# Optimization experiments

Measured on AMD Instinct MI355X. Metric: run time of the kernel, lower is better.

The kernel has to match this reference:

```python
import jax, jax.numpy as jnp
import numpy as np
import math

K_SLOTS = 64
DIM = 512
HEADS = 8
HEAD_DIM = DIM // HEADS
EPS = 1e-20
LN_EPS = 1e-5
SQRT_DIM = 1.0 / math.sqrt(HEAD_DIM)


def layernorm(x, g, b):
    mu = jnp.mean(x, axis=-1, keepdims=True)
    var = jnp.var(x, axis=-1, keepdims=True)
    return (x - mu) * jax.lax.rsqrt(var + LN_EPS) * g + b


def setup_inputs() -> dict:
    key = jax.random.key(0)
    ks = jax.random.split(key, 8)
    B, T = 8, 8192
    lim = 1.0 / math.sqrt(DIM)
    return {
        "X": jax.random.normal(ks[0], (B, T, DIM), jnp.float32),
        "slots_w": jax.random.normal(ks[1], (K_SLOTS, DIM), jnp.float32),
        "g_slots": jnp.ones((DIM,), jnp.float32),
        "b_slots": jnp.zeros((DIM,), jnp.float32),
        "Wk": jax.random.uniform(ks[2], (DIM, DIM), jnp.float32, -lim, lim),
        "bk": jax.random.uniform(ks[3], (DIM,), jnp.float32, -lim, lim),
        "Wv": jax.random.uniform(ks[4], (DIM, DIM), jnp.float32, -lim, lim),
        "bv": jax.random.uniform(ks[5], (DIM,), jnp.float32, -lim, lim),
        "g_after": jnp.ones((DIM,), jnp.float32),
        "b_after": jnp.zeros((DIM,), jnp.float32),
    }


def reference(X, slots_w, g_slots, b_slots, Wk, bk, Wv, bv, g_after, b_after):
    B, T, D = X.shape
    # slots -> queries, shared across batch: (K, D) -> (H, K, hd)
    S = layernorm(slots_w, g_slots, b_slots)
    Q = S.reshape(K_SLOTS, HEADS, HEAD_DIM).transpose(1, 0, 2)  # (H, K, hd)
    # key/value projections, head split: (B, T, D) -> (B, H, T, hd)
    Kx = (X @ Wk.T + bk).reshape(B, T, HEADS, HEAD_DIM).transpose(0, 2, 1, 3)
    V = (X @ Wv.T + bv).reshape(B, T, HEADS, HEAD_DIM).transpose(0, 2, 1, 3)
    # attention logits (B, H, K, T), scale = 1/sqrt(head_dim)
    A = jnp.einsum("hkd,bhsd->bhks", Q, Kx) * SQRT_DIM
    # softmax over the SLOT axis (k), then renormalize by row-sum over s
    W = jax.nn.softmax(A, axis=-2)
    C = jnp.sum(W, axis=-1, keepdims=True)  # (B, H, K, 1)
    A = W / (C + EPS)
    S_hat = jnp.einsum("bhks,bhsd->bhkd", A, V)  # (B, H, K, hd)
    S_hat = S_hat.transpose(0, 2, 1, 3).reshape(B, K_SLOTS, D)
    return layernorm(S_hat, g_after, b_after)
```

## Files before the change

### kernel.cpp

```cpp
#include <hip/hip_runtime.h>
#include <hip/hip_bf16.h>
#include <math.h>

typedef unsigned short ushort_t;
typedef unsigned int u32;

constexpr int D  = 512;
constexpr int T  = 8192;
constexpr int B  = 8;
constexpr int H  = 8;
constexpr int KS = 64;
constexpr int HD = 64;
constexpr float SCALE = 0.125f;
constexpr float LNEPS = 1e-5f;
constexpr float EPS   = 1e-20f;

constexpr int TC  = 128;
constexpr int CPB = 2;

constexpr size_t OFF_S    = 0;
constexpr size_t OFF_BQ   = 32768;
constexpr size_t OFF_SACC = 33280;
constexpr size_t OFF_CACC = 295424;
constexpr size_t OFF_WB2  = 299520;
constexpr size_t OFF_XB   = 561664;
constexpr size_t WS_NEED  = (OFF_XB + (size_t)B*T*D/2) * 4;

typedef __attribute__((ext_vector_type(8))) short bf16x8;
typedef __attribute__((ext_vector_type(4))) float f32x4;
typedef __attribute__((ext_vector_type(4))) unsigned short us4;

typedef const __attribute__((address_space(1))) u32* gas_ptr;
typedef __attribute__((address_space(3))) u32* las_ptr;

__device__ __forceinline__ void gload16(const void* g, void* l) {
  __builtin_amdgcn_global_load_lds((gas_ptr)g, (las_ptr)l, 16, 0, 0);
}

__device__ __forceinline__ ushort_t f2bf(float x) {
  __hip_bfloat16 t = __float2bfloat16(x);
  return *(ushort_t*)&t;
}

__device__ __forceinline__ u32 pk2bf(float x, float y) {
  __hip_bfloat162 t = __float22bfloat162_rn(make_float2(x, y));
  return *(u32*)&t;
}

__device__ __forceinline__ bf16x8 cvt8(f32x4 a, f32x4 b) {
  union { bf16x8 v; u32 u[4]; } r;
  r.u[0] = pk2bf(a.x, a.y); r.u[1] = pk2bf(a.z, a.w);
  r.u[2] = pk2bf(b.x, b.y); r.u[3] = pk2bf(b.z, b.w);
  return r.v;
}

__global__ void ln_slots_kernel(const float* __restrict__ slots_w,
                                const float* __restrict__ g, const float* __restrict__ b,
                                float* __restrict__ S) {
  __shared__ float red[8];
  int k = blockIdx.x;
  int tid = threadIdx.x;
  float x0 = slots_w[k*D + tid];
  float x1 = slots_w[k*D + tid + 256];
  float s1 = x0 + x1, s2 = x0*x0 + x1*x1;
  for (int off = 32; off; off >>= 1) { s1 += __shfl_xor(s1, off); s2 += __shfl_xor(s2, off); }
  if ((tid & 63) == 0) { red[tid >> 6] = s1; red[4 + (tid >> 6)] = s2; }
  __syncthreads();
  s1 = red[0] + red[1] + red[2] + red[3];
  s2 = red[4] + red[5] + red[6] + red[7];
  float mu = s1 / D;
  float var = s2 / D - mu * mu;
  float rs = rsqrtf(var + LNEPS);
  S[k*D + tid]       = (x0 - mu) * rs * g[tid]       + b[tid];
  S[k*D + tid + 256] = (x1 - mu) * rs * g[tid + 256] + b[tid + 256];
}

__global__ void weff_kernel(const float* __restrict__ S, const float* __restrict__ Wk,
                            ushort_t* __restrict__ Wb2) {
  int gid = blockIdx.x * 256 + threadIdx.x;
  int in = gid & 511;
  int hk = gid >> 9;
  int h = hk >> 6, k = hk & 63;
  const float* srow = S + k*D + h*HD;
  const float* wcol = Wk + (size_t)(h*HD)*D + in;
  float acc = 0.f;
  #pragma unroll 8
  for (int d = 0; d < HD; ++d) acc += srow[d] * wcol[(size_t)d*D];
  Wb2[(size_t)(h*128 + k)*D + in] = f2bf(acc * SCALE);
}

__global__ void bq_kernel(const float* __restrict__ S, const float* __restrict__ bk,
                          float* __restrict__ bq) {
  int hk = blockIdx.x * 256 + threadIdx.x;
  int h = hk >> 6, k = hk & 63;
  float acc = 0.f;
  for (int d = 0; d < HD; ++d) acc += S[k*D + h*HD + d] * bk[h*HD + d];
  bq[hk] = acc * SCALE;
}

__global__ void wvcopy_kernel(const float* __restrict__ Wv, ushort_t* __restrict__ Wb2) {
  int gid = blockIdx.x * 256 + threadIdx.x;
  int in = gid & 511;
  int hd = gid >> 9;
  int h = hd >> 6, d = hd & 63;
  Wb2[(size_t)(h*128 + 64 + d)*D + in] = f2bf(Wv[(size_t)hd*D + in]);
}

__global__ void zero_kernel(float* __restrict__ p, int n) {
  int gid = blockIdx.x * 256 + threadIdx.x;
  if (gid < n) p[gid] = 0.f;
}

__global__ void xcvt_kernel(const float* __restrict__ X, ushort_t* __restrict__ Xb) {
  size_t i = ((size_t)blockIdx.x * 256 + threadIdx.x) * 8;
  f32x4 a = *(const f32x4*)(X + i);
  f32x4 b = *(const f32x4*)(X + i + 4);
  *(bf16x8*)(Xb + i) = cvt8(a, b);
}

__global__ __launch_bounds__(256, 4) void main_kernel_bf16(
    const ushort_t* __restrict__ Xb, const ushort_t* __restrict__ Wb2,
    const float* __restrict__ bq, const float* __restrict__ bv,
    float* __restrict__ Sacc, float* __restrict__ Cacc) {
  __shared__ __align__(16) char smem[34816];
  ushort_t* A_lds = (ushort_t*)smem;
  ushort_t* B_lds = (ushort_t*)(smem + 8192);
  ushort_t* W_lds = (ushort_t*)smem;
  ushort_t* V_lds = (ushort_t*)(smem + 17408);

  const int tid  = threadIdx.x;
  const int lane = tid & 63, w = tid >> 6;
  const int wm = w & 1, wn = w >> 1;
  const int m16 = lane & 15, q = lane >> 4;
  const int kq = q ^ ((m16 >> 1) & 3);

  const int id = blockIdx.x;
  const int h  = (id >> 3) & 7;
  const int cg = (id & 7) | ((id >> 6) << 3);
  const int bh = (cg >> 5) * H + h;

  f32x4 acc2[4] = {};
  float csum[4] = {0.f, 0.f, 0.f, 0.f};

  for (int cc = 0; cc < CPB; ++cc) {
    const ushort_t* Xc = Xb + (size_t)(cg * CPB + cc) * TC * D;
    f32x4 acc[4][4] = {};

    for (int kb = 0; kb < D; kb += 32) {
      __syncthreads();
      #pragma unroll
      for (int m = 0; m < 2; ++m) {
        int li = tid + m * 256;
        int row = li >> 2;
        int kc = (li & 3) ^ ((row >> 1) & 3);
        gload16(Xc + (size_t)row * D + kb + kc * 8, A_lds + (size_t)li * 8);
      }
      #pragma unroll
      for (int m = 0; m < 2; ++m) {
        int li = tid + m * 256;
        int col = li >> 2;
        int kc = (li & 3) ^ ((col >> 1) & 3);
        gload16(Wb2 + (size_t)(h * 128 + col) * D + kb + kc * 8, B_lds + (size_t)li * 8);
      }
      __syncthreads();
      bf16x8 af[4], bfv[4];
      #pragma unroll
      for (int i = 0; i < 4; ++i)
        af[i] = *(const bf16x8*)(A_lds + (size_t)(((wm*64 + i*16 + m16) << 2) | kq) * 8);
      #pragma unroll
      for (int j = 0; j < 4; ++j)
        bfv[j] = *(const bf16x8*)(B_lds + (size_t)(((wn*64 + j*16 + m16) << 2) | kq) * 8);
      #pragma unroll
      for (int i = 0; i < 4; ++i)
        #pragma unroll
        for (int j = 0; j < 4; ++j)
          acc[i][j] = __builtin_amdgcn_mfma_f32_16x16x32_bf16(af[i], bfv[j], acc[i][j], 0, 0, 0);
    }
    __syncthreads();

    if (wn == 0) {
      float bqv[4];
      #pragma unroll
      for (int j = 0; j < 4; ++j) bqv[j] = bq[h * KS + j * 16 + m16];
      #pragma unroll
      for (int i = 0; i < 4; ++i) {
        us4 wp[4];
        #pragma unroll
        for (int r = 0; r < 4; ++r) {
          float v0 = acc[i][0][r] + bqv[0];
          float v1 = acc[i][1][r] + bqv[1];
          float v2 = acc[i][2][r] + bqv[2];
          float v3 = acc[i][3][r] + bqv[3];
          float mx = fmaxf(fmaxf(v0, v1), fmaxf(v2, v3));
          mx = fmaxf(mx, __shfl_xor(mx, 1));
          mx = fmaxf(mx, __shfl_xor(mx, 2));
          mx = fmaxf(mx, __shfl_xor(mx, 4));
          mx = fmaxf(mx, __shfl_xor(mx, 8));
          v0 = __expf(v0 - mx); v1 = __expf(v1 - mx);
          v2 = __expf(v2 - mx); v3 = __expf(v3 - mx);
          float s = v0 + v1 + v2 + v3;
          s += __shfl_xor(s, 1); s += __shfl_xor(s, 2);
          s += __shfl_xor(s, 4); s += __shfl_xor(s, 8);
          float inv = __builtin_amdgcn_rcpf(s);
          v0 *= inv; v1 *= inv; v2 *= inv; v3 *= inv;
          csum[0] += v0; csum[1] += v1; csum[2] += v2; csum[3] += v3;
          wp[0][r] = f2bf(v0); wp[1][r] = f2bf(v1);
          wp[2][r] = f2bf(v2); wp[3][r] = f2bf(v3);
        }
        #pragma unroll
        for (int j = 0; j < 4; ++j)
          *(us4*)(W_lds + (j * 16 + m16) * 136 + wm * 64 + i * 16 + q * 4) = wp[j];
      }
    } else {
      float bvv[4];
      #pragma unroll
      for (int j = 0; j < 4; ++j) bvv[j] = bv[h * HD + j * 16 + m16];
      #pragma unroll
      for (int i = 0; i < 4; ++i) {
        #pragma unroll
        for (int j = 0; j < 4; ++j) {
          us4 pk;
          pk.x = f2bf(acc[i][j][0] + bvv[j]);
          pk.y = f2bf(acc[i][j][1] + bvv[j]);
          pk.z = f2bf(acc[i][j][2] + bvv[j]);
          pk.w = f2bf(acc[i][j][3] + bvv[j]);
          *(us4*)(V_lds + (j * 16 + m16) * 136 + wm * 64 + i * 16 + q * 4) = pk;
        }
      }
    }
    __syncthreads();

    #pragma unroll
    for (int kk = 0; kk < 4; ++kk) {
      bf16x8 a = *(const bf16x8*)(W_lds + (w * 16 + m16) * 136 + kk * 32 + q * 8);
      #pragma unroll
      for (int j = 0; j < 4; ++j) {
        bf16x8 bb = *(const bf16x8*)(V_lds + (j * 16 + m16) * 136 + kk * 32 + q * 8);
        acc2[j] = __builtin_amdgcn_mfma_f32_16x16x32_bf16(a, bb, acc2[j], 0, 0, 0);
      }
    }
  }

  float* Sb = Sacc + (size_t)bh * KS * HD;
  #pragma unroll
  for (int j = 0; j < 4; ++j)
    #pragma unroll
    for (int r = 0; r < 4; ++r)
      atomicAdd(Sb + (w * 16 + q * 4 + r) * HD + j * 16 + m16, acc2[j][r]);

  if (wn == 0) {
    #pragma unroll
    for (int j = 0; j < 4; ++j) {
      float c = csum[j];
      c += __shfl_xor(c, 16);
      c += __shfl_xor(c, 32);
      if (q == 0) atomicAdd(Cacc + (size_t)bh * KS + j * 16 + m16, c);
    }
  }
}

__global__ __launch_bounds__(256, 3) void main_kernel_f32(
    const float* __restrict__ X, const ushort_t* __restrict__ Wb2,
    const float* __restrict__ bq, const float* __restrict__ bv,
    float* __restrict__ Sacc, float* __restrict__ Cacc) {
  __shared__ __align__(16) char smem[34816];
  float*    A_lds = (float*)smem;
  ushort_t* B_lds = (ushort_t*)(smem + 16384);
  ushort_t* W_lds = (ushort_t*)smem;
  ushort_t* V_lds = (ushort_t*)(smem + 17408);

  const int tid  = threadIdx.x;
  const int lane = tid & 63, w = tid >> 6;
  const int wm = w & 1, wn = w >> 1;
  const int m16 = lane & 15, q = lane >> 4;

  const int id = blockIdx.x;
  const int h  = (id >> 3) & 7;
  const int cg = (id & 7) | ((id >> 6) << 3);
  const int bh = (cg >> 5) * H + h;

  f32x4 acc2[4] = {};
  float csum[4] = {0.f, 0.f, 0.f, 0.f};

  for (int cc = 0; cc < CPB; ++cc) {
    const float* Xc = X + (size_t)(cg * CPB + cc) * TC * D;
    f32x4 acc[4][4] = {};
    for (int kb = 0; kb < D; kb += 32) {
      __syncthreads();
      #pragma unroll
      for (int m = 0; m < 4; ++m) {
        int li = tid + m * 256;
        int row = li >> 3, c = li & 7;
        gload16(Xc + (size_t)row * D + kb + c * 4, A_lds + (size_t)li * 4);
      }
      #pragma unroll
      for (int m = 0; m < 2; ++m) {
        int li = tid + m * 256;
        int col = li >> 2, c = li & 3;
        gload16(Wb2 + (size_t)(h * 128 + col) * D + kb + c * 8, B_lds + (size_t)li * 8);
      }
      __syncthreads();
      bf16x8 af[4], bfv[4];
      #pragma unroll
      for (int i = 0; i < 4; ++i) {
        const f32x4* ap = (const f32x4*)(A_lds + (wm * 64 + i * 16 + m16) * 32 + q * 8);
        af[i] = cvt8(ap[0], ap[1]);
      }
      #pragma unroll
      for (int j = 0; j < 4; ++j)
        bfv[j] = *(const bf16x8*)(B_lds + (wn * 64 + j * 16 + m16) * 32 + q * 8);
      #pragma unroll
      for (int i = 0; i < 4; ++i)
        #pragma unroll
        for (int j = 0; j < 4; ++j)
          acc[i][j] = __builtin_amdgcn_mfma_f32_16x16x32_bf16(af[i], bfv[j], acc[i][j], 0, 0, 0);
    }
    __syncthreads();

    if (wn == 0) {
      float bqv[4];
      #pragma unroll
      for (int j = 0; j < 4; ++j) bqv[j] = bq[h * KS + j * 16 + m16];
      #pragma unroll
      for (int i = 0; i < 4; ++i) {
        us4 wp[4];
        #pragma unroll
        for (int r = 0; r < 4; ++r) {
          float v0 = acc[i][0][r] + bqv[0];
          float v1 = acc[i][1][r] + bqv[1];
          float v2 = acc[i][2][r] + bqv[2];
          float v3 = acc[i][3][r] + bqv[3];
          float mx = fmaxf(fmaxf(v0, v1), fmaxf(v2, v3));
          mx = fmaxf(mx, __shfl_xor(mx, 1));
          mx = fmaxf(mx, __shfl_xor(mx, 2));
          mx = fmaxf(mx, __shfl_xor(mx, 4));
          mx = fmaxf(mx, __shfl_xor(mx, 8));
          v0 = __expf(v0 - mx); v1 = __expf(v1 - mx);
          v2 = __expf(v2 - mx); v3 = __expf(v3 - mx);
          float s = v0 + v1 + v2 + v3;
          s += __shfl_xor(s, 1); s += __shfl_xor(s, 2);
          s += __shfl_xor(s, 4); s += __shfl_xor(s, 8);
          float inv = __builtin_amdgcn_rcpf(s);
          v0 *= inv; v1 *= inv; v2 *= inv; v3 *= inv;
          csum[0] += v0; csum[1] += v1; csum[2] += v2; csum[3] += v3;
          wp[0][r] = f2bf(v0); wp[1][r] = f2bf(v1);
          wp[2][r] = f2bf(v2); wp[3][r] = f2bf(v3);
        }
        #pragma unroll
        for (int j = 0; j < 4; ++j)
          *(us4*)(W_lds + (j * 16 + m16) * 136 + wm * 64 + i * 16 + q * 4) = wp[j];
      }
    } else {
      float bvv[4];
      #pragma unroll
      for (int j = 0; j < 4; ++j) bvv[j] = bv[h * HD + j * 16 + m16];
      #pragma unroll
      for (int i = 0; i < 4; ++i) {
        #pragma unroll
        for (int j = 0; j < 4; ++j) {
          us4 pk;
          pk.x = f2bf(acc[i][j][0] + bvv[j]);
          pk.y = f2bf(acc[i][j][1] + bvv[j]);
          pk.z = f2bf(acc[i][j][2] + bvv[j]);
          pk.w = f2bf(acc[i][j][3] + bvv[j]);
          *(us4*)(V_lds + (j * 16 + m16) * 136 + wm * 64 + i * 16 + q * 4) = pk;
        }
      }
    }
    __syncthreads();

    #pragma unroll
    for (int kk = 0; kk < 4; ++kk) {
      bf16x8 a = *(const bf16x8*)(W_lds + (w * 16 + m16) * 136 + kk * 32 + q * 8);
      #pragma unroll
      for (int j = 0; j < 4; ++j) {
        bf16x8 bb = *(const bf16x8*)(V_lds + (j * 16 + m16) * 136 + kk * 32 + q * 8);
        acc2[j] = __builtin_amdgcn_mfma_f32_16x16x32_bf16(a, bb, acc2[j], 0, 0, 0);
      }
    }
  }

  float* Sb = Sacc + (size_t)bh * KS * HD;
  #pragma unroll
  for (int j = 0; j < 4; ++j)
    #pragma unroll
    for (int r = 0; r < 4; ++r)
      atomicAdd(Sb + (w * 16 + q * 4 + r) * HD + j * 16 + m16, acc2[j][r]);

  if (wn == 0) {
    #pragma unroll
    for (int j = 0; j < 4; ++j) {
      float c = csum[j];
      c += __shfl_xor(c, 16);
      c += __shfl_xor(c, 32);
      if (q == 0) atomicAdd(Cacc + (size_t)bh * KS + j * 16 + m16, c);
    }
  }
}

__global__ void finalize_kernel(const float* __restrict__ Sacc, const float* __restrict__ Cacc,
                                const float* __restrict__ g, const float* __restrict__ bb,
                                float* __restrict__ out) {
  __shared__ float red[8];
  int bk_ = blockIdx.x;
  int b = bk_ >> 6, k = bk_ & 63;
  int tid = threadIdx.x;
  float v[2];
  #pragma unroll
  for (int m = 0; m < 2; ++m) {
    int d = tid + m*256;
    int h = d >> 6, dd = d & 63;
    float c = Cacc[((size_t)b*H + h)*KS + k];
    v[m] = Sacc[(((size_t)b*H + h)*KS + k)*HD + dd] / (c + EPS);
  }
  float s1 = v[0] + v[1], s2 = v[0]*v[0] + v[1]*v[1];
  for (int off = 32; off; off >>= 1) { s1 += __shfl_xor(s1, off); s2 += __shfl_xor(s2, off); }
  if ((tid & 63) == 0) { red[tid >> 6] = s1; red[4 + (tid >> 6)] = s2; }
  __syncthreads();
  s1 = red[0] + red[1] + red[2] + red[3];
  s2 = red[4] + red[5] + red[6] + red[7];
  float mu = s1 / D;
  float var = s2 / D - mu * mu;
  float rs = rsqrtf(var + LNEPS);
  #pragma unroll
  for (int m = 0; m < 2; ++m) {
    int d = tid + m*256;
    out[(size_t)bk_*D + d] = (v[m] - mu) * rs * g[d] + bb[d];
  }
}

extern "C" void kernel_launch(void* const* d_in, const int* in_sizes, int n_in,
                              void* d_out, int out_size, void* d_ws, size_t ws_size,
                              hipStream_t stream) {
  const float* X       = (const float*)d_in[0];
  const float* slots_w = (const float*)d_in[1];
  const float* g_slots = (const float*)d_in[2];
  const float* b_slots = (const float*)d_in[3];
  const float* Wk      = (const float*)d_in[4];
  const float* bk      = (const float*)d_in[5];
  const float* Wv      = (const float*)d_in[6];
  const float* bv      = (const float*)d_in[7];
  const float* g_after = (const float*)d_in[8];
  const float* b_after = (const float*)d_in[9];
  float* ws   = (float*)d_ws;
  float* S    = ws + OFF_S;
  float* bq   = ws + OFF_BQ;
  float* Sacc = ws + OFF_SACC;
  float* Cacc = ws + OFF_CACC;
  ushort_t* Wb2 = (ushort_t*)(ws + OFF_WB2);
  ushort_t* Xb  = (ushort_t*)(ws + OFF_XB);
  float* out  = (float*)d_out;

  hipLaunchKernelGGL(ln_slots_kernel, dim3(64), dim3(256), 0, stream, slots_w, g_slots, b_slots, S);
  hipLaunchKernelGGL(weff_kernel, dim3(1024), dim3(256), 0, stream, S, Wk, Wb2);
  hipLaunchKernelGGL(bq_kernel, dim3(2), dim3(256), 0, stream, S, bk, bq);
  hipLaunchKernelGGL(wvcopy_kernel, dim3(1024), dim3(256), 0, stream, Wv, Wb2);
  hipLaunchKernelGGL(zero_kernel, dim3(1040), dim3(256), 0, stream, Sacc, 266240);
  if (ws_size >= WS_NEED) {
    hipLaunchKernelGGL(xcvt_kernel, dim3(16384), dim3(256), 0, stream, X, Xb);
    hipLaunchKernelGGL(main_kernel_bf16, dim3(2048), dim3(256), 0, stream,
                       Xb, Wb2, bq, bv, Sacc, Cacc);
  } else {
    hipLaunchKernelGGL(main_kernel_f32, dim3(2048), dim3(256), 0, stream,
                       X, Wb2, bq, bv, Sacc, Cacc);
  }
  hipLaunchKernelGGL(finalize_kernel, dim3(B * KS), dim3(256), 0, stream,
                     Sacc, Cacc, g_after, b_after, out);
}
```

Measured before the change: 416.5 us.

## Keep a bf16 X tile in LDS and process all heads per block

Removes the separate X-to-bf16 conversion pass. A new 512-thread kernel loads each 128-token chunk of fp32 X once, converts it to bf16 into a large swizzled LDS tile (about 144KB of dynamic shared memory), and loops over all 8 heads. B fragments are read directly from global memory with register double-buffering, so X is no longer re-read once per head. The cost is one block per CU with no overlap between the initial X load and compute, plus more barriers in the per-head W·V stage.

New measurement: 416.5 us. Within noise of the previous version (-0.0%).

```diff
diff --git a/kernel.cpp b/kernel.cpp
--- a/kernel.cpp
+++ b/kernel.cpp
@@ -15,16 +15,15 @@
 constexpr float LNEPS = 1e-5f;
 constexpr float EPS   = 1e-20f;
 
-constexpr int TC  = 128;
-constexpr int CPB = 2;
+constexpr int TC = 128;
 
 constexpr size_t OFF_S    = 0;
 constexpr size_t OFF_BQ   = 32768;
 constexpr size_t OFF_SACC = 33280;
 constexpr size_t OFF_CACC = 295424;
 constexpr size_t OFF_WB2  = 299520;
-constexpr size_t OFF_XB   = 561664;
-constexpr size_t WS_NEED  = (OFF_XB + (size_t)B*T*D/2) * 4;
+
+constexpr int MAIN_LDS = 147456;
 
 typedef __attribute__((ext_vector_type(8))) short bf16x8;
 typedef __attribute__((ext_vector_type(4))) float f32x4;
@@ -111,20 +110,174 @@
   if (gid < n) p[gid] = 0.f;
 }
 
-__global__ void xcvt_kernel(const float* __restrict__ X, ushort_t* __restrict__ Xb) {
-  size_t i = ((size_t)blockIdx.x * 256 + threadIdx.x) * 8;
-  f32x4 a = *(const f32x4*)(X + i);
-  f32x4 b = *(const f32x4*)(X + i + 4);
-  *(bf16x8*)(Xb + i) = cvt8(a, b);
-}
-
-__global__ __launch_bounds__(256, 4) void main_kernel_bf16(
-    const ushort_t* __restrict__ Xb, const ushort_t* __restrict__ Wb2,
+__global__ __launch_bounds__(512, 2) void main_kernel_ah(
+    const float* __restrict__ X, const ushort_t* __restrict__ Wb2,
+    const float* __restrict__ bq, const float* __restrict__ bv,
+    float* __restrict__ Sacc, float* __restrict__ Cacc) {
+  extern __shared__ __align__(16) char smem[];
+  ushort_t* X_lds = (ushort_t*)smem;
+  ushort_t* W_lds = (ushort_t*)(smem + 131072);
+  ushort_t* V_lds = (ushort_t*)(smem + 139264);
+
+  const int tid = threadIdx.x;
+  const int w = tid >> 6, lane = tid & 63;
+  const int m16 = lane & 15, q = lane >> 4;
+  const int th = w & 1, cqq = w >> 1;
+  const int bid = blockIdx.x;
+  const int bb = bid >> 6;
+  const float* Xc = X + (size_t)bid * TC * D;
+
+  #pragma unroll
+  for (int m = 0; m < 16; ++m) {
+    int C = m * 512 + tid;
+    int token = C >> 6, c = C & 63;
+    const f32x4* src = (const f32x4*)(Xc + (size_t)C * 8);
+    f32x4 a = src[0], b2 = src[1];
+    *(bf16x8*)(X_lds + ((size_t)token * 64 + (c ^ (token & 7))) * 8) = cvt8(a, b2);
+  }
+  __syncthreads();
+
+  const int hh_my = cqq >> 1;
+  const int isV   = cqq & 1;
+
+  for (int p = 0; p < 4; ++p) {
+    f32x4 acc[4][4] = {};
+    const ushort_t* Bp = Wb2 + ((size_t)((p * 2 + hh_my) * 128 + isV * 64 + m16)) * D + q * 8;
+    bf16x8 bnx[4];
+    #pragma unroll
+    for (int j = 0; j < 4; ++j) bnx[j] = *(const bf16x8*)(Bp + (size_t)j * 16 * D);
+    #pragma unroll 2
+    for (int it = 0; it < 16; ++it) {
+      bf16x8 bc[4];
+      #pragma unroll
+      for (int j = 0; j < 4; ++j) bc[j] = bnx[j];
+      if (it < 15) {
+        #pragma unroll
+        for (int j = 0; j < 4; ++j)
+          bnx[j] = *(const bf16x8*)(Bp + (it + 1) * 32 + (size_t)j * 16 * D);
+      }
+      bf16x8 af[4];
+      #pragma unroll
+      for (int i = 0; i < 4; ++i) {
+        int token = th * 64 + i * 16 + m16;
+        af[i] = *(const bf16x8*)(X_lds + ((size_t)token * 64 + ((it * 4 + q) ^ (token & 7))) * 8);
+      }
+      #pragma unroll
+      for (int i = 0; i < 4; ++i)
+        #pragma unroll
+        for (int j = 0; j < 4; ++j)
+          acc[i][j] = __builtin_amdgcn_mfma_f32_16x16x32_bf16(af[i], bc[j], acc[i][j], 0, 0, 0);
+    }
+
+    for (int hh = 0; hh < 2; ++hh) {
+      const int head = p * 2 + hh;
+      const int bh = bb * 8 + head;
+      const bool mine = (hh_my == hh);
+      us4 pk[4][4];
+      if (mine) {
+        if (!isV) {
+          float bqv[4];
+          #pragma unroll
+          for (int j = 0; j < 4; ++j) bqv[j] = bq[head * 64 + j * 16 + m16];
+          float cs0 = 0.f, cs1 = 0.f, cs2 = 0.f, cs3 = 0.f;
+          #pragma unroll
+          for (int i = 0; i < 4; ++i) {
+            #pragma unroll
+            for (int r = 0; r < 4; ++r) {
+              float v0 = acc[i][0][r] + bqv[0];
+              float v1 = acc[i][1][r] + bqv[1];
+              float v2 = acc[i][2][r] + bqv[2];
+              float v3 = acc[i][3][r] + bqv[3];
+              float mx = fmaxf(fmaxf(v0, v1), fmaxf(v2, v3));
+              mx = fmaxf(mx, __shfl_xor(mx, 1));
+              mx = fmaxf(mx, __shfl_xor(mx, 2));
+              mx = fmaxf(mx, __shfl_xor(mx, 4));
+              mx = fmaxf(mx, __shfl_xor(mx, 8));
+              v0 = __expf(v0 - mx); v1 = __expf(v1 - mx);
+              v2 = __expf(v2 - mx); v3 = __expf(v3 - mx);
+              float s = v0 + v1 + v2 + v3;
+              s += __shfl_xor(s, 1); s += __shfl_xor(s, 2);
+              s += __shfl_xor(s, 4); s += __shfl_xor(s, 8);
+              float inv = __builtin_amdgcn_rcpf(s);
+              v0 *= inv; v1 *= inv; v2 *= inv; v3 *= inv;
+              cs0 += v0; cs1 += v1; cs2 += v2; cs3 += v3;
+              pk[i][0][r] = f2bf(v0); pk[i][1][r] = f2bf(v1);
+              pk[i][2][r] = f2bf(v2); pk[i][3][r] = f2bf(v3);
+            }
+          }
+          cs0 += __shfl_xor(cs0, 16); cs0 += __shfl_xor(cs0, 32);
+          cs1 += __shfl_xor(cs1, 16); cs1 += __shfl_xor(cs1, 32);
+          cs2 += __shfl_xor(cs2, 16); cs2 += __shfl_xor(cs2, 32);
+          cs3 += __shfl_xor(cs3, 16); cs3 += __shfl_xor(cs3, 32);
+          if (q == 0) {
+            atomicAdd(Cacc + (size_t)bh * KS +  0 + m16, cs0);
+            atomicAdd(Cacc + (size_t)bh * KS + 16 + m16, cs1);
+            atomicAdd(Cacc + (size_t)bh * KS + 32 + m16, cs2);
+            atomicAdd(Cacc + (size_t)bh * KS + 48 + m16, cs3);
+          }
+        } else {
+          float bvv[4];
+          #pragma unroll
+          for (int j = 0; j < 4; ++j) bvv[j] = bv[head * 64 + j * 16 + m16];
+          #pragma unroll
+          for (int i = 0; i < 4; ++i)
+            #pragma unroll
+            for (int j = 0; j < 4; ++j) {
+              pk[i][j][0] = f2bf(acc[i][j][0] + bvv[j]);
+              pk[i][j][1] = f2bf(acc[i][j][1] + bvv[j]);
+              pk[i][j][2] = f2bf(acc[i][j][2] + bvv[j]);
+              pk[i][j][3] = f2bf(acc[i][j][3] + bvv[j]);
+            }
+        }
+      }
+
+      f32x4 acc2[2] = {};
+      #pragma unroll
+      for (int half = 0; half < 2; ++half) {
+        __syncthreads();
+        if (mine && th == half) {
+          ushort_t* dst = isV ? V_lds : W_lds;
+          #pragma unroll
+          for (int i = 0; i < 4; ++i)
+            #pragma unroll
+            for (int j = 0; j < 4; ++j) {
+              int rowv = j * 16 + m16;
+              int tc = i * 2 + (q >> 1);
+              *(us4*)(dst + ((size_t)rowv * 8 + (tc ^ (rowv & 7))) * 8 + (q & 1) * 4) = pk[i][j];
+            }
+        }
+        __syncthreads();
+        #pragma unroll
+        for (int ks = 0; ks < 2; ++ks) {
+          int tcc = ks * 4 + q;
+          int sl = (w & 3) * 16 + m16;
+          bf16x8 a2 = *(const bf16x8*)(W_lds + ((size_t)sl * 8 + (tcc ^ (m16 & 7))) * 8);
+          #pragma unroll
+          for (int jj = 0; jj < 2; ++jj) {
+            int dm = (w >> 2) * 32 + jj * 16 + m16;
+            bf16x8 b2v = *(const bf16x8*)(V_lds + ((size_t)dm * 8 + (tcc ^ (m16 & 7))) * 8);
+            acc2[jj] = __builtin_amdgcn_mfma_f32_16x16x32_bf16(a2, b2v, acc2[jj], 0, 0, 0);
+          }
+        }
+      }
+      float* Sb = Sacc + (size_t)bh * KS * HD;
+      #pragma unroll
+      for (int jj = 0; jj < 2; ++jj)
+        #pragma unroll
+        for (int r = 0; r < 4; ++r)
+          atomicAdd(Sb + ((w & 3) * 16 + q * 4 + r) * HD + (w >> 2) * 32 + jj * 16 + m16,
+                    acc2[jj][r]);
+    }
+  }
+}
+
+__global__ __launch_bounds__(256, 3) void main_kernel_f32(
+    const float* __restrict__ X, const ushort_t* __restrict__ Wb2,
     const float* __restrict__ bq, const float* __restrict__ bv,
     float* __restrict__ Sacc, float* __restrict__ Cacc) {
   __shared__ __align__(16) char smem[34816];
-  ushort_t* A_lds = (ushort_t*)smem;
-  ushort_t* B_lds = (ushort_t*)(smem + 8192);
+  float*    A_lds = (float*)smem;
+  ushort_t* B_lds = (ushort_t*)(smem + 16384);
   ushort_t* W_lds = (ushort_t*)smem;
   ushort_t* V_lds = (ushort_t*)(smem + 17408);
 
@@ -132,7 +285,6 @@
   const int lane = tid & 63, w = tid >> 6;
   const int wm = w & 1, wn = w >> 1;
   const int m16 = lane & 15, q = lane >> 4;
-  const int kq = q ^ ((m16 >> 1) & 3);
 
   const int id = blockIdx.x;
   const int h  = (id >> 3) & 7;
@@ -142,34 +294,33 @@
   f32x4 acc2[4] = {};
   float csum[4] = {0.f, 0.f, 0.f, 0.f};
 
-  for (int cc = 0; cc < CPB; ++cc) {
-    const ushort_t* Xc = Xb + (size_t)(cg * CPB + cc) * TC * D;
+  for (int cc = 0; cc < 2; ++cc) {
+    const float* Xc = X + (size_t)(cg * 2 + cc) * 128 * D;
     f32x4 acc[4][4] = {};
-
     for (int kb = 0; kb < D; kb += 32) {
       __syncthreads();
       #pragma unroll
+      for (int m = 0; m < 4; ++m) {
+        int li = tid + m * 256;
+        int row = li >> 3, c = li & 7;
+        gload16(Xc + (size_t)row * D + kb + c * 4, A_lds + (size_t)li * 4);
+      }
+      #pragma unroll
       for (int m = 0; m < 2; ++m) {
         int li = tid + m * 256;
-        int row = li >> 2;
-        int kc = (li & 3) ^ ((row >> 1) & 3);
-        gload16(Xc + (size_t)row * D + kb + kc * 8, A_lds + (size_t)li * 8);
-      }
-      #pragma unroll
-      for (int m = 0; m < 2; ++m) {
-        int li = tid + m * 256;
-        int col = li >> 2;
-        int kc = (li & 3) ^ ((col >> 1) & 3);
-        gload16(Wb2 + (size_t)(h * 128 + col) * D + kb + kc * 8, B_lds + (size_t)li * 8);
+        int col = li >> 2, c = li & 3;
+        gload16(Wb2 + (size_t)(h * 128 + col) * D + kb + c * 8, B_lds + (size_t)li * 8);
       }
       __syncthreads();
       bf16x8 af[4], bfv[4];
       #pragma unroll
-      for (int i = 0; i < 4; ++i)
-        af[i] = *(const bf16x8*)(A_lds + (size_t)(((wm*64 + i*16 + m16) << 2) | kq) * 8);
+      for (int i = 0; i < 4; ++i) {
+        const f32x4* ap = (const f32x4*)(A_lds + (wm * 64 + i * 16 + m16) * 32 + q * 8);
+        af[i] = cvt8(ap[0], ap[1]);
+      }
       #pragma unroll
       for (int j = 0; j < 4; ++j)
-        bfv[j] = *(const bf16x8*)(B_lds + (size_t)(((wn*64 + j*16 + m16) << 2) | kq) * 8);
+        bfv[j] = *(const bf16x8*)(B_lds + (wn * 64 + j * 16 + m16) * 32 + q * 8);
       #pragma unroll
       for (int i = 0; i < 4; ++i)
         #pragma unroll
@@ -214,158 +365,18 @@
     } else {
       float bvv[4];
       #pragma unroll
-      for (int j = 0; j < 4; ++j) bvv[j] = bv[h * HD + j * 16 + m16];
-      #pragma unroll
-      for (int i = 0; i < 4; ++i) {
+      for (int j = 0; j < 4; ++j) bvv[j] = bv[h * HD + (j * 16 + m16 < 64 ? j * 16 + m16 : 0)];
+      #pragma unroll
+      for (int i = 0; i < 4; ++i)
         #pragma unroll
         for (int j = 0; j < 4; ++j) {
-          us4 pk;
-          pk.x = f2bf(acc[i][j][0] + bvv[j]);
-          pk.y = f2bf(acc[i][j][1] + bvv[j]);
-          pk.z = f2bf(acc[i][j][2] + bvv[j]);
-          pk.w = f2bf(acc[i][j][3] + bvv[j]);
-          *(us4*)(V_lds + (j * 16 + m16) * 136 + wm * 64 + i * 16 + q * 4) = pk;
+          us4 pkk;
+          pkk[0] = f2bf(acc[i][j][0] + bvv[j]);
+          pkk[1] = f2bf(acc[i][j][1] + bvv[j]);
+          pkk[2] = f2bf(acc[i][j][2] + bvv[j]);
+          pkk[3] = f2bf(acc[i][j][3] + bvv[j]);
+          *(us4*)(V_lds + (j * 16 + m16) * 136 + wm * 64 + i * 16 + q * 4) = pkk;
         }
-      }
-    }
-    __syncthreads();
-
-    #pragma unroll
-    for (int kk = 0; kk < 4; ++kk) {
-      bf16x8 a = *(const bf16x8*)(W_lds + (w * 16 + m16) * 136 + kk * 32 + q * 8);
-      #pragma unroll
-      for (int j = 0; j < 4; ++j) {
-        bf16x8 bb = *(const bf16x8*)(V_lds + (j * 16 + m16) * 136 + kk * 32 + q * 8);
-        acc2[j] = __builtin_amdgcn_mfma_f32_16x16x32_bf16(a, bb, acc2[j], 0, 0, 0);
-      }
-    }
-  }
-
-  float* Sb = Sacc + (size_t)bh * KS * HD;
-  #pragma unroll
-  for (int j = 0; j < 4; ++j)
-    #pragma unroll
-    for (int r = 0; r < 4; ++r)
-      atomicAdd(Sb + (w * 16 + q * 4 + r) * HD + j * 16 + m16, acc2[j][r]);
-
-  if (wn == 0) {
-    #pragma unroll
-    for (int j = 0; j < 4; ++j) {
-      float c = csum[j];
-      c += __shfl_xor(c, 16);
-      c += __shfl_xor(c, 32);
-      if (q == 0) atomicAdd(Cacc + (size_t)bh * KS + j * 16 + m16, c);
-    }
-  }
-}
-
-__global__ __launch_bounds__(256, 3) void main_kernel_f32(
-    const float* __restrict__ X, const ushort_t* __restrict__ Wb2,
-    const float* __restrict__ bq, const float* __restrict__ bv,
-    float* __restrict__ Sacc, float* __restrict__ Cacc) {
-  __shared__ __align__(16) char smem[34816];
-  float*    A_lds = (float*)smem;
-  ushort_t* B_lds = (ushort_t*)(smem + 16384);
-  ushort_t* W_lds = (ushort_t*)smem;
-  ushort_t* V_lds = (ushort_t*)(smem + 17408);
-
-  const int tid  = threadIdx.x;
-  const int lane = tid & 63, w = tid >> 6;
-  const int wm = w & 1, wn = w >> 1;
-  const int m16 = lane & 15, q = lane >> 4;
-
-  const int id = blockIdx.x;
-  const int h  = (id >> 3) & 7;
-  const int cg = (id & 7) | ((id >> 6) << 3);
-  const int bh = (cg >> 5) * H + h;
-
-  f32x4 acc2[4] = {};
-  float csum[4] = {0.f, 0.f, 0.f, 0.f};
-
-  for (int cc = 0; cc < CPB; ++cc) {
-    const float* Xc = X + (size_t)(cg * CPB + cc) * TC * D;
-    f32x4 acc[4][4] = {};
-    for (int kb = 0; kb < D; kb += 32) {
-      __syncthreads();
-      #pragma unroll
-      for (int m = 0; m < 4; ++m) {
-        int li = tid + m * 256;
-        int row = li >> 3, c = li & 7;
-        gload16(Xc + (size_t)row * D + kb + c * 4, A_lds + (size_t)li * 4);
-      }
-      #pragma unroll
-      for (int m = 0; m < 2; ++m) {
-        int li = tid + m * 256;
-        int col = li >> 2, c = li & 3;
-        gload16(Wb2 + (size_t)(h * 128 + col) * D + kb + c * 8, B_lds + (size_t)li * 8);
-      }
-      __syncthreads();
-      bf16x8 af[4], bfv[4];
-      #pragma unroll
-      for (int i = 0; i < 4; ++i) {
-        const f32x4* ap = (const f32x4*)(A_lds + (wm * 64 + i * 16 + m16) * 32 + q * 8);
-        af[i] = cvt8(ap[0], ap[1]);
-      }
-      #pragma unroll
-      for (int j = 0; j < 4; ++j)
-        bfv[j] = *(const bf16x8*)(B_lds + (wn * 64 + j * 16 + m16) * 32 + q * 8);
-      #pragma unroll
-      for (int i = 0; i < 4; ++i)
-        #pragma unroll
-        for (int j = 0; j < 4; ++j)
-          acc[i][j] = __builtin_amdgcn_mfma_f32_16x16x32_bf16(af[i], bfv[j], acc[i][j], 0, 0, 0);
-    }
-    __syncthreads();
-
-    if (wn == 0) {
-      float bqv[4];
-      #pragma unroll
-      for (int j = 0; j < 4; ++j) bqv[j] = bq[h * KS + j * 16 + m16];
-      #pragma unroll
-      for (int i = 0; i < 4; ++i) {
-        us4 wp[4];
-        #pragma unroll
-        for (int r = 0; r < 4; ++r) {
-          float v0 = acc[i][0][r] + bqv[0];
-          float v1 = acc[i][1][r] + bqv[1];
-          float v2 = acc[i][2][r] + bqv[2];
-          float v3 = acc[i][3][r] + bqv[3];
-          float mx = fmaxf(fmaxf(v0, v1), fmaxf(v2, v3));
-          mx = fmaxf(mx, __shfl_xor(mx, 1));
-          mx = fmaxf(mx, __shfl_xor(mx, 2));
-          mx = fmaxf(mx, __shfl_xor(mx, 4));
-          mx = fmaxf(mx, __shfl_xor(mx, 8));
-          v0 = __expf(v0 - mx); v1 = __expf(v1 - mx);
-          v2 = __expf(v2 - mx); v3 = __expf(v3 - mx);
-          float s = v0 + v1 + v2 + v3;
-          s += __shfl_xor(s, 1); s += __shfl_xor(s, 2);
-          s += __shfl_xor(s, 4); s += __shfl_xor(s, 8);
-          float inv = __builtin_amdgcn_rcpf(s);
-          v0 *= inv; v1 *= inv; v2 *= inv; v3 *= inv;
-          csum[0] += v0; csum[1] += v1; csum[2] += v2; csum[3] += v3;
-          wp[0][r] = f2bf(v0); wp[1][r] = f2bf(v1);
-          wp[2][r] = f2bf(v2); wp[3][r] = f2bf(v3);
-        }
-        #pragma unroll
-        for (int j = 0; j < 4; ++j)
-          *(us4*)(W_lds + (j * 16 + m16) * 136 + wm * 64 + i * 16 + q * 4) = wp[j];
-      }
-    } else {
-      float bvv[4];
-      #pragma unroll
-      for (int j = 0; j < 4; ++j) bvv[j] = bv[h * HD + j * 16 + m16];
-      #pragma unroll
-      for (int i = 0; i < 4; ++i) {
-        #pragma unroll
-        for (int j = 0; j < 4; ++j) {
-          us4 pk;
-          pk.x = f2bf(acc[i][j][0] + bvv[j]);
-          pk.y = f2bf(acc[i][j][1] + bvv[j]);
-          pk.z = f2bf(acc[i][j][2] + bvv[j]);
-          pk.w = f2bf(acc[i][j][3] + bvv[j]);
-          *(us4*)(V_lds + (j * 16 + m16) * 136 + wm * 64 + i * 16 + q * 4) = pk;
-        }
-      }
     }
     __syncthreads();
 
@@ -448,7 +459,6 @@
   float* Sacc = ws + OFF_SACC;
   float* Cacc = ws + OFF_CACC;
   ushort_t* Wb2 = (ushort_t*)(ws + OFF_WB2);
-  ushort_t* Xb  = (ushort_t*)(ws + OFF_XB);
   float* out  = (float*)d_out;
 
   hipLaunchKernelGGL(ln_slots_kernel, dim3(64), dim3(256), 0, stream, slots_w, g_slots, b_slots, S);
@@ -456,10 +466,13 @@
   hipLaunchKernelGGL(bq_kernel, dim3(2), dim3(256), 0, stream, S, bk, bq);
   hipLaunchKernelGGL(wvcopy_kernel, dim3(1024), dim3(256), 0, stream, Wv, Wb2);
   hipLaunchKernelGGL(zero_kernel, dim3(1040), dim3(256), 0, stream, Sacc, 266240);
-  if (ws_size >= WS_NEED) {
-    hipLaunchKernelGGL(xcvt_kernel, dim3(16384), dim3(256), 0, stream, X, Xb);
-    hipLaunchKernelGGL(main_kernel_bf16, dim3(2048), dim3(256), 0, stream,
-                       Xb, Wb2, bq, bv, Sacc, Cacc);
+
+  hipError_t attr_ok = hipFuncSetAttribute(
+      reinterpret_cast<const void*>(main_kernel_ah),
+      hipFuncAttributeMaxDynamicSharedMemorySize, MAIN_LDS);
+  if (attr_ok == hipSuccess) {
+    hipLaunchKernelGGL(main_kernel_ah, dim3(B * T / TC), dim3(512), MAIN_LDS, stream,
+                       X, Wb2, bq, bv, Sacc, Cacc);
   } else {
     hipLaunchKernelGGL(main_kernel_f32, dim3(2048), dim3(256), 0, stream,
                        X, Wb2, bq, bv, Sacc, Cacc);
```
